# Kernel tuning notes

Measured on AMD Instinct MI355X. Metric: run time of the kernel, lower is better.

## Reference

```python
import jax, jax.numpy as jnp
import numpy as np

T, N, E = 4, 40000, 640000
D_IN, D_HID, D_OUT, NCLASS = 256, 256, 256, 2
NEG = 0.2  # leaky_relu negative slope (both GATv2 internal and outer activations)


def segment_softmax(logits, seg, n):
    m = jax.ops.segment_max(logits, seg, num_segments=n)
    ex = jnp.exp(logits - m[seg])
    s = jax.ops.segment_sum(ex, seg, num_segments=n)
    return ex / s[seg]


def gatv2(x, src, dst, Wl, Wr, bl, br, att, bias, n):
    # PyG GATv2Conv, heads=1, concat: lin_l on source, lin_r on target,
    # e = att . leaky_relu(xl_j + xr_i), softmax over incoming edges of i,
    # out_i = sum_j alpha_ij * xl_j + bias. Self-loops already appended.
    xl = x @ Wl + bl                                   # [n, C]
    xr = x @ Wr + br                                   # [n, C]
    e = jax.nn.leaky_relu(xl[src] + xr[dst], NEG)      # [E', C]
    alpha = segment_softmax(e @ att, dst, n)           # [E']
    out = jax.ops.segment_sum(alpha[:, None] * xl[src], dst, num_segments=n)
    return out + bias


def setup_inputs() -> dict:
    key = jax.random.key(0)
    ks = jax.random.split(key, 18)
    w = lambda k, shape, fan: (jax.random.normal(k, shape, dtype=jnp.float32) / np.sqrt(fan)).astype(jnp.float32)
    return {
        "fts": jax.random.normal(ks[0], (T, N, D_IN), dtype=jnp.float32),
        "graph": jax.random.randint(ks[1], (T, 2, E), 0, N, dtype=jnp.int32),
        "Wl0": w(ks[2], (D_IN, D_HID), D_IN),
        "Wr0": w(ks[3], (D_IN, D_HID), D_IN),
        "bl0": jnp.zeros((D_HID,), jnp.float32),
        "br0": jnp.zeros((D_HID,), jnp.float32),
        "att0": w(ks[4], (D_HID,), D_HID),
        "b0": jnp.zeros((D_HID,), jnp.float32),
        "Wl1": w(ks[5], (D_HID, D_OUT), D_HID),
        "Wr1": w(ks[6], (D_HID, D_OUT), D_HID),
        "bl1": jnp.zeros((D_OUT,), jnp.float32),
        "br1": jnp.zeros((D_OUT,), jnp.float32),
        "att1": w(ks[7], (D_OUT,), D_OUT),
        "b1": jnp.zeros((D_OUT,), jnp.float32),
        "W_lin": w(ks[8], (D_OUT, NCLASS), D_OUT),
        "b_lin": jnp.zeros((NCLASS,), jnp.float32),
        "time_steps": T,
    }


def reference(fts, graph, Wl0, Wr0, bl0, br0, att0, b0,
              Wl1, Wr1, bl1, br1, att1, b1, W_lin, b_lin, time_steps):
    n = fts.shape[1]
    loops = jnp.arange(n, dtype=graph.dtype)
    # PyG add_self_loops=True: append (i, i) edges per graph used.
    src0 = jnp.concatenate([graph[0, 0], loops])
    dst0 = jnp.concatenate([graph[0, 1], loops])
    # BUG-faithful: only timestep 0 survives (y = y[0]) but the last layer
    # uses G from the LAST timestep; timesteps 1..T-1 are dead compute.
    srcL = jnp.concatenate([graph[time_steps - 1, 0], loops])
    dstL = jnp.concatenate([graph[time_steps - 1, 1], loops])
    y = jax.nn.leaky_relu(gatv2(fts[0], src0, dst0, Wl0, Wr0, bl0, br0, att0, b0, n), NEG)
    y = jax.nn.leaky_relu(gatv2(y, srcL, dstL, Wl1, Wr1, bl1, br1, att1, b1, n), NEG)
    # dropout is identity in eval mode
    y = y @ W_lin + b_lin
    return jax.nn.log_softmax(y, axis=1)  # [N, nclass]
```

## Files before the change

kernel.cpp:

```cpp
#include <hip/hip_runtime.h>
#include <hip/hip_bf16.h>
#include <math.h>

#define NEG 0.2f
#define NB_MAX 256
#define CAP 5120

typedef float f32x4 __attribute__((ext_vector_type(4)));
typedef _Float16 f16;
typedef _Float16 f16x2 __attribute__((ext_vector_type(2)));
typedef _Float16 f16x8 __attribute__((ext_vector_type(8)));

#if defined(__has_builtin)
#if __has_builtin(__builtin_amdgcn_fdot2)
#define HAVE_FDOT2 1
#endif
#endif

typedef __attribute__((address_space(3))) void as3_void;
typedef __attribute__((address_space(1))) const void as1_void;

__device__ __forceinline__ void gl_lds16(const void* g, void* l) {
    __builtin_amdgcn_global_load_lds((as1_void*)g, (as3_void*)l, 16, 0, 0);
}

__global__ __launch_bounds__(256) void convert_w2(const float* __restrict__ Wl0,
                                                  const float* __restrict__ Wr0,
                                                  const float* __restrict__ Wl1,
                                                  const float* __restrict__ Wr1,
                                                  _Float16* __restrict__ Wt,
                                                  int* __restrict__ bkt_next, int nb2) {
    int l = blockIdx.y;
    int idx = blockIdx.x * blockDim.x + threadIdx.x;
    int n = idx >> 8, k = idx & 255;
    const float* Wl = l ? Wl1 : Wl0;
    const float* Wr = l ? Wr1 : Wr0;
    float v = (n < 256) ? Wl[k * 256 + n] : Wr[k * 256 + (n - 256)];
    Wt[(size_t)l * 512 * 256 + idx] = (_Float16)v;
    if (blockIdx.x == 0 && l == 0)
        for (int i = threadIdx.x; i < nb2; i += 256) bkt_next[i] = 0;
}

__device__ __forceinline__ void stage16(const _Float16* __restrict__ src,
                                        int row_base, int row_max, int k0,
                                        char* lds, int tid) {
#pragma unroll
    for (int q = 0; q < 2; ++q) {
        int off = q * 4096 + tid * 16;
        int row = off >> 6;
        int slot = (off >> 4) & 3;
        int se = slot ^ (row & 3);
        int grow = row_base + row;
        if (grow > row_max) grow = row_max;
        gl_lds16(src + (size_t)grow * 256 + k0 + se * 8,
                 lds + q * 4096 + (tid >> 6) * 1024);
    }
}

__device__ __forceinline__ void stage16_f32(const float* __restrict__ X,
                                            int row_base, int row_max, int k0,
                                            char* lds, int tid) {
#pragma unroll
    for (int u = 0; u < 4; ++u) {
        int unit = u * 256 + tid;
        int r = unit >> 3, hu = unit & 7;
        int slot = hu >> 1, sub = (hu & 1) * 8;
        int se = slot ^ (r & 3);
        int grow = row_base + r;
        if (grow > row_max) grow = row_max;
        float4 v = *(const float4*)(X + (size_t)grow * 256 + k0 + se * 8 + (hu & 1) * 4);
        f16x2 p0 = {(f16)v.x, (f16)v.y};
        f16x2 p1 = {(f16)v.z, (f16)v.w};
        uint2 w;
        w.x = __builtin_bit_cast(unsigned, p0);
        w.y = __builtin_bit_cast(unsigned, p1);
        *(uint2*)(lds + r * 64 + slot * 16 + sub) = w;
    }
}

template <int SRC>
__device__ __forceinline__ void gemm_body(char* smem, int b,
                                          const float* __restrict__ Xf,
                                          const _Float16* __restrict__ X16,
                                          const _Float16* __restrict__ Wt,
                                          const float* __restrict__ bl,
                                          const float* __restrict__ br,
                                          _Float16* __restrict__ Af,
                                          _Float16* __restrict__ Bf, int M) {
    int Mb = (M + 127) >> 7;
    int cx = b & 7, rr = b >> 3;
    int m_blk = (rr >> 2) * 8 + cx;
    int n_blk = rr & 3;
    if (m_blk >= Mb) return;
    int tid = threadIdx.x;
    int wave = tid >> 6, lane = tid & 63;
    int m0 = m_blk * 128;
    int wr = wave >> 1, wc = wave & 1;
    int r15 = lane & 15, c = lane >> 4;

    f32x4 acc[4][4];
#pragma unroll
    for (int mf = 0; mf < 4; ++mf)
#pragma unroll
        for (int nf = 0; nf < 4; ++nf) acc[mf][nf] = (f32x4){0.f, 0.f, 0.f, 0.f};

    auto stageX = [&](int k0, char* dst) {
        if constexpr (SRC == 0) stage16_f32(Xf, m0, M - 1, k0, dst, tid);
        else                    stage16(X16, m0, M - 1, k0, dst, tid);
    };

    stageX(0, smem);
    stage16(Wt, n_blk * 128, 511, 0, smem + 8192, tid);
    __syncthreads();

    for (int t = 0; t < 8; ++t) {
        int buf = t & 1;
        if (t < 7) {
            char* nb2 = smem + (buf ^ 1) * 16384;
            stageX((t + 1) * 32, nb2);
            stage16(Wt, n_blk * 128, 511, (t + 1) * 32, nb2 + 8192, tid);
        }
        const char* At = smem + buf * 16384;
        const char* Bt = At + 8192;
        f16x8 af[4], bf[4];
#pragma unroll
        for (int f = 0; f < 4; ++f) {
            int ar = wr * 64 + f * 16 + r15;
            af[f] = *(const f16x8*)(At + ar * 64 + ((c ^ (ar & 3)) << 4));
            int br_ = wc * 64 + f * 16 + r15;
            bf[f] = *(const f16x8*)(Bt + br_ * 64 + ((c ^ (br_ & 3)) << 4));
        }
#pragma unroll
        for (int mf = 0; mf < 4; ++mf)
#pragma unroll
            for (int nf = 0; nf < 4; ++nf)
                acc[mf][nf] = __builtin_amdgcn_mfma_f32_16x16x32_f16(af[mf], bf[nf], acc[mf][nf], 0, 0, 0);
        __syncthreads();
    }

    int q4 = (lane >> 4) * 4;
#pragma unroll
    for (int nf = 0; nf < 4; ++nf) {
        int n_abs = n_blk * 128 + wc * 64 + nf * 16 + r15;
        bool left = n_abs < 256;
        float bb = left ? bl[n_abs] : br[n_abs - 256];
        int col = n_abs & 255;
#pragma unroll
        for (int mf = 0; mf < 4; ++mf) {
            int rowb = m0 + wr * 64 + mf * 16 + q4;
#pragma unroll
            for (int j = 0; j < 4; ++j) {
                int row = rowb + j;
                if (row < M) {
                    float v = acc[mf][nf][j] + bb;
                    if (left) Af[(size_t)row * 256 + col] = (_Float16)v;
                    else      Bf[(size_t)row * 256 + col] = (_Float16)v;
                }
            }
        }
    }
}

__global__ __launch_bounds__(256) void binA(const int* __restrict__ src0,
                                            const int* __restrict__ dst0,
                                            const int* __restrict__ src1,
                                            const int* __restrict__ dst1,
                                            int Ereal, int EP, int nb,
                                            int* __restrict__ bkt_next,
                                            unsigned* __restrict__ bucketBuf) {
    __shared__ int hist[NB_MAX], base[NB_MAX], ofs[NB_MAX];
    int l = blockIdx.y;
    for (int i = threadIdx.x; i < nb; i += 256) hist[i] = 0;
    __syncthreads();
    const int* src = l ? src1 : src0;
    const int* dst = l ? dst1 : dst0;
    int c0 = blockIdx.x * 4096;
    int dcache[16];
#pragma unroll
    for (int k = 0; k < 16; ++k) {
        int i = c0 + k * 256 + threadIdx.x;
        int d = -1;
        if (i < EP) d = (i < Ereal) ? dst[i] : (i - Ereal);
        dcache[k] = d;
        if (d >= 0) atomicAdd(&hist[d >> 8], 1);
    }
    __syncthreads();
    for (int i = threadIdx.x; i < nb; i += 256) {
        base[i] = hist[i] ? atomicAdd(&bkt_next[l * nb + i], hist[i]) : 0;
        ofs[i] = 0;
    }
    __syncthreads();
#pragma unroll
    for (int k = 0; k < 16; ++k) {
        int i = c0 + k * 256 + threadIdx.x;
        int d = dcache[k];
        if (d >= 0) {
            int s = (i < Ereal) ? src[i] : (i - Ereal);
            int bk = d >> 8;
            int pos = base[bk] + atomicAdd(&ofs[bk], 1);
            bucketBuf[(size_t)(l * nb + bk) * CAP + pos] = (unsigned)s | ((unsigned)(d & 255) << 16);
        }
    }
}

__global__ __launch_bounds__(256) void binB_gemm0(const unsigned* __restrict__ bucketBuf,
                                                  const int* __restrict__ bkt_cnt,
                                                  int nb, int N,
                                                  int* __restrict__ beg,
                                                  int* __restrict__ end_,
                                                  unsigned short* __restrict__ csr16,
                                                  const float* __restrict__ Xf,
                                                  const _Float16* __restrict__ Wt,
                                                  const float* __restrict__ bl,
                                                  const float* __restrict__ br,
                                                  _Float16* __restrict__ Af,
                                                  _Float16* __restrict__ Bf, int M) {
    __shared__ char smem[32768];
    int blk = blockIdx.x;
    if (blk < 2 * nb) {
        int* hist = (int*)smem;
        int* sh   = (int*)(smem + 1024);
        int* nxt  = (int*)(smem + 2048);
        int l = blk / nb, b = blk % nb, t = threadIdx.x;
        int cnt = bkt_cnt[l * nb + b];
        const unsigned* buf = bucketBuf + (size_t)(l * nb + b) * CAP;
        unsigned short* csrL = csr16 + (size_t)l * nb * CAP;
        hist[t] = 0;
        __syncthreads();
        for (int i = t; i < cnt; i += 256)
            atomicAdd(&hist[buf[i] >> 16], 1);
        __syncthreads();
        int h = hist[t];
        sh[t] = h;
        __syncthreads();
        for (int o = 1; o < 256; o <<= 1) {
            int x = (t >= o) ? sh[t - o] : 0;
            __syncthreads();
            sh[t] += x;
            __syncthreads();
        }
        int excl = sh[t] - h;
        nxt[t] = excl;
        int d = b * 256 + t;
        if (d < N) {
            beg[(size_t)l * N + d] = b * CAP + excl;
            end_[(size_t)l * N + d] = b * CAP + excl + h;
        }
        __syncthreads();
        for (int i = t; i < cnt; i += 256) {
            unsigned v = buf[i];
            int pos = b * CAP + atomicAdd(&nxt[v >> 16], 1);
            csrL[pos] = (unsigned short)(v & 0xFFFFu);
        }
        return;
    }
    gemm_body<0>(smem, blk - 2 * nb, Xf, nullptr, Wt, bl, br, Af, Bf, M);
}

__global__ __launch_bounds__(256) void mfma_gemm1(const _Float16* __restrict__ X16,
                                                  const _Float16* __restrict__ Wt,
                                                  const float* __restrict__ bl,
                                                  const float* __restrict__ br,
                                                  _Float16* __restrict__ Af,
                                                  _Float16* __restrict__ Bf, int M) {
    __shared__ char smem[32768];
    gemm_body<1>(smem, blockIdx.x, nullptr, X16, Wt, bl, br, Af, Bf, M);
}

template <int MODE>
__global__ __launch_bounds__(256) void gat_node(const _Float16* __restrict__ xl,
                                                const _Float16* __restrict__ xr,
                                                const int* __restrict__ beg_,
                                                const int* __restrict__ end_,
                                                const unsigned short* __restrict__ csr,
                                                const float* __restrict__ att,
                                                const float* __restrict__ bias,
                                                _Float16* __restrict__ y16,
                                                const float* __restrict__ Wlin,
                                                const float* __restrict__ blin,
                                                float* __restrict__ out, int n) {
    int wid = (int)((blockIdx.x * (size_t)blockDim.x + threadIdx.x) >> 6);
    int lane = threadIdx.x & 63;
    if (wid >= n) return;
    int g = lane >> 5, li = lane & 31;
    int beg = beg_[wid], end = end_[wid];

    f16x8 xr8 = ((const f16x8*)(xr + (size_t)wid * 256))[li];
    float4 t0 = ((const float4*)att)[li * 2];
    float4 t1 = ((const float4*)att)[li * 2 + 1];
    f16x2 t01 = {(f16)t0.x, (f16)t0.y}, t23 = {(f16)t0.z, (f16)t0.w};
    f16x2 t45 = {(f16)t1.x, (f16)t1.y}, t67 = {(f16)t1.z, (f16)t1.w};
    const f16 ng = (f16)NEG;
    const f16x8 n8 = {ng, ng, ng, ng, ng, ng, ng, ng};

    float m = -INFINITY, ssum = 0.f;
    float acc[8] = {0.f, 0.f, 0.f, 0.f, 0.f, 0.f, 0.f, 0.f};

    auto step = [&](f16x8 a, bool valid) {
        f16x8 v = a + xr8;
        f16x8 lk = __builtin_elementwise_max(v, v * n8);
#ifdef HAVE_FDOT2
        f16x2 q;
        q[0] = lk[0]; q[1] = lk[1];
        float dot = __builtin_amdgcn_fdot2(q, t01, 0.f, false);
        q[0] = lk[2]; q[1] = lk[3];
        dot = __builtin_amdgcn_fdot2(q, t23, dot, false);
        q[0] = lk[4]; q[1] = lk[5];
        dot = __builtin_amdgcn_fdot2(q, t45, dot, false);
        q[0] = lk[6]; q[1] = lk[7];
        dot = __builtin_amdgcn_fdot2(q, t67, dot, false);
#else
        float dot = (float)lk[0] * (float)t01[0] + (float)lk[1] * (float)t01[1] +
                    (float)lk[2] * (float)t23[0] + (float)lk[3] * (float)t23[1] +
                    (float)lk[4] * (float)t45[0] + (float)lk[5] * (float)t45[1] +
                    (float)lk[6] * (float)t67[0] + (float)lk[7] * (float)t67[1];
#endif
#pragma unroll
        for (int off = 16; off > 0; off >>= 1) dot += __shfl_xor(dot, off);
        if (valid) {
            if (dot > m + 8.f) {
                float sc = __expf(m - dot);
                ssum = ssum * sc + 1.f;
#pragma unroll
                for (int i = 0; i < 8; ++i) acc[i] = acc[i] * sc + (float)a[i];
                m = dot;
            } else {
                float p = __expf(dot - m);
                ssum += p;
#pragma unroll
                for (int i = 0; i < 8; ++i) acc[i] += p * (float)a[i];
            }
        }
    };

    int j = beg;
    for (; j + 16 <= end; j += 16) {
        f16x8 a[8];
#pragma unroll
        for (int u = 0; u < 8; ++u) {
            int s = csr[j + 2 * u + g];
            a[u] = ((const f16x8*)(xl + (size_t)s * 256))[li];
        }
#pragma unroll
        for (int u = 0; u < 8; ++u) step(a[u], true);
    }
    if (j + 8 <= end) {
        f16x8 a[4];
#pragma unroll
        for (int u = 0; u < 4; ++u) {
            int s = csr[j + 2 * u + g];
            a[u] = ((const f16x8*)(xl + (size_t)s * 256))[li];
        }
#pragma unroll
        for (int u = 0; u < 4; ++u) step(a[u], true);
        j += 8;
    }
    for (; j < end; j += 2) {
        int e = j + g;
        int s = csr[e < end ? e : end - 1];
        f16x8 a = ((const f16x8*)(xl + (size_t)s * 256))[li];
        step(a, e < end);
    }

    float m_o = __shfl_xor(m, 32);
    float s_o = __shfl_xor(ssum, 32);
    float ms = fmaxf(m, m_o);
    float wa = __expf(m - ms), wb = __expf(m_o - ms);
    float inv = 1.f / (ssum * wa + s_o * wb);
    float4 bb0 = ((const float4*)bias)[li * 2];
    float4 bb1 = ((const float4*)bias)[li * 2 + 1];
    float bbv[8] = {bb0.x, bb0.y, bb0.z, bb0.w, bb1.x, bb1.y, bb1.z, bb1.w};
    float o8[8];
#pragma unroll
    for (int i = 0; i < 8; ++i) {
        float ao = __shfl_xor(acc[i], 32);
        float o = (acc[i] * wa + ao * wb) * inv + bbv[i];
        o8[i] = o > 0.f ? o : NEG * o;
    }

    if (MODE == 0) {
        if (g == 0) {
            f16x8 w;
#pragma unroll
            for (int i = 0; i < 8; ++i) w[i] = (f16)o8[i];
            ((f16x8*)(y16 + (size_t)wid * 256))[li] = w;
        }
    } else {
        float z0 = 0.f, z1 = 0.f;
#pragma unroll
        for (int p = 0; p < 4; ++p) {
            float4 q = ((const float4*)Wlin)[li * 4 + p];
            z0 += o8[2 * p] * q.x + o8[2 * p + 1] * q.z;
            z1 += o8[2 * p] * q.y + o8[2 * p + 1] * q.w;
        }
#pragma unroll
        for (int off = 16; off > 0; off >>= 1) {
            z0 += __shfl_xor(z0, off);
            z1 += __shfl_xor(z1, off);
        }
        if (lane == 0) {
            z0 += blin[0];
            z1 += blin[1];
            float mx = fmaxf(z0, z1);
            float lse = mx + logf(expf(z0 - mx) + expf(z1 - mx));
            out[(size_t)wid * 2 + 0] = z0 - lse;
            out[(size_t)wid * 2 + 1] = z1 - lse;
        }
    }
}

extern "C" void kernel_launch(void* const* d_in, const int* in_sizes, int n_in,
                              void* d_out, int out_size, void* d_ws, size_t ws_size,
                              hipStream_t stream) {
    const float* fts   = (const float*)d_in[0];
    const int*   graph = (const int*)d_in[1];
    const float* Wl0 = (const float*)d_in[2];
    const float* Wr0 = (const float*)d_in[3];
    const float* bl0 = (const float*)d_in[4];
    const float* br0 = (const float*)d_in[5];
    const float* att0 = (const float*)d_in[6];
    const float* b0  = (const float*)d_in[7];
    const float* Wl1 = (const float*)d_in[8];
    const float* Wr1 = (const float*)d_in[9];
    const float* bl1 = (const float*)d_in[10];
    const float* br1 = (const float*)d_in[11];
    const float* att1 = (const float*)d_in[12];
    const float* b1  = (const float*)d_in[13];
    const float* Wlin = (const float*)d_in[14];
    const float* blin = (const float*)d_in[15];

    int N = out_size / 2;
    long T = in_sizes[0] / ((long)N * 256);
    long E = in_sizes[1] / (2 * T);
    int EP = (int)E + N;
    int nb = (N + 255) / 256;

    char* ws = (char*)d_ws;
    size_t off = 0;
    auto alloc = [&](size_t bytes) -> void* {
        void* p = ws + off;
        off += (bytes + 255) & ~(size_t)255;
        return p;
    };
    _Float16* Af  = (_Float16*)alloc((size_t)N * 256 * 2);
    _Float16* Bf  = (_Float16*)alloc((size_t)N * 256 * 2);
    _Float16* Y16 = (_Float16*)alloc((size_t)N * 256 * 2);
    _Float16* Wt  = (_Float16*)alloc((size_t)2 * 512 * 256 * 2);
    int* beg      = (int*)alloc((size_t)2 * N * 4);
    int* end_     = (int*)alloc((size_t)2 * N * 4);
    unsigned short* csr16 = (unsigned short*)alloc((size_t)2 * nb * CAP * 2);
    unsigned* bucketBuf = (unsigned*)alloc((size_t)2 * nb * CAP * 4);
    int* bkt_next = (int*)alloc((size_t)2 * nb * 4);
    (void)ws_size; (void)n_in;

    int Mb = (N + 127) / 128;
    int gemm_blocks = ((Mb + 7) / 8) * 8 * 4;
    dim3 chunk_grid((EP + 4095) / 4096, 2);
    int node_blocks = (N + 3) / 4;

    const int* src0 = graph;
    const int* dst0 = graph + E;
    const int* srcL = graph + (T - 1) * 2 * E;
    const int* dstL = graph + (T - 1) * 2 * E + E;

    convert_w2<<<dim3(512, 2), 256, 0, stream>>>(Wl0, Wr0, Wl1, Wr1, Wt, bkt_next, 2 * nb);
    binA<<<chunk_grid, 256, 0, stream>>>(src0, dst0, srcL, dstL, (int)E, EP, nb,
                                         bkt_next, bucketBuf);
    binB_gemm0<<<2 * nb + gemm_blocks, 256, 0, stream>>>(bucketBuf, bkt_next, nb, N,
                                                         beg, end_, csr16,
                                                         fts, Wt, bl0, br0, Af, Bf, N);
    gat_node<0><<<node_blocks, 256, 0, stream>>>(Af, Bf, beg, end_, csr16, att0, b0,
                                                 Y16, nullptr, nullptr, nullptr, N);
    mfma_gemm1<<<gemm_blocks, 256, 0, stream>>>(Y16, Wt + (size_t)512 * 256,
                                                bl1, br1, Af, Bf, N);
    gat_node<1><<<node_blocks, 256, 0, stream>>>(Af, Bf, beg + N, end_ + N,
                                                 csr16 + (size_t)nb * CAP, att1, b1,
                                                 nullptr, Wlin, blin, (float*)d_out, N);
}
```

Baseline: 232.6 us.

## Split layer-0 aggregation and overlap its tail with layer-1 GEMM

Layer-0 node aggregation is split into two launches. The second launch co-schedules the remaining nodes with layer-1 GEMM tiles over rows already finished, and a separate launch handles the leftover GEMM tiles. Layer-1 outputs go to new buffers so the GEMM no longer overwrites xl/xr while aggregation still reads them. The weight conversion is merged into the binning kernel and the counter zeroing moves to a memset. Non-temporal loads and stores are also used for xr and y16. This adds launches and workspace, and the co-scheduled kernel mixes block types with different resource needs.

```diff
diff --git a/kernel.cpp b/kernel.cpp
--- a/kernel.cpp
+++ b/kernel.cpp
@@ -10,6 +10,7 @@
 typedef _Float16 f16;
 typedef _Float16 f16x2 __attribute__((ext_vector_type(2)));
 typedef _Float16 f16x8 __attribute__((ext_vector_type(8)));
+typedef unsigned u32x4 __attribute__((ext_vector_type(4)));
 
 #if defined(__has_builtin)
 #if __has_builtin(__builtin_amdgcn_fdot2)
@@ -24,21 +25,12 @@
     __builtin_amdgcn_global_load_lds((as1_void*)g, (as3_void*)l, 16, 0, 0);
 }
 
-__global__ __launch_bounds__(256) void convert_w2(const float* __restrict__ Wl0,
-                                                  const float* __restrict__ Wr0,
-                                                  const float* __restrict__ Wl1,
-                                                  const float* __restrict__ Wr1,
-                                                  _Float16* __restrict__ Wt,
-                                                  int* __restrict__ bkt_next, int nb2) {
-    int l = blockIdx.y;
-    int idx = blockIdx.x * blockDim.x + threadIdx.x;
-    int n = idx >> 8, k = idx & 255;
-    const float* Wl = l ? Wl1 : Wl0;
-    const float* Wr = l ? Wr1 : Wr0;
-    float v = (n < 256) ? Wl[k * 256 + n] : Wr[k * 256 + (n - 256)];
-    Wt[(size_t)l * 512 * 256 + idx] = (_Float16)v;
-    if (blockIdx.x == 0 && l == 0)
-        for (int i = threadIdx.x; i < nb2; i += 256) bkt_next[i] = 0;
+__device__ __forceinline__ f16x8 nt_load8(const _Float16* p) {
+    u32x4 v = __builtin_nontemporal_load((const u32x4*)p);
+    return __builtin_bit_cast(f16x8, v);
+}
+__device__ __forceinline__ void nt_store8(_Float16* p, f16x8 w) {
+    __builtin_nontemporal_store(__builtin_bit_cast(u32x4, w), (u32x4*)p);
 }
 
 __device__ __forceinline__ void stage16(const _Float16* __restrict__ src,
@@ -79,7 +71,7 @@
 }
 
 template <int SRC>
-__device__ __forceinline__ void gemm_body(char* smem, int b,
+__device__ __forceinline__ void gemm_body(char* smem, int b, int m_base, int m_tiles,
                                           const float* __restrict__ Xf,
                                           const _Float16* __restrict__ X16,
                                           const _Float16* __restrict__ Wt,
@@ -87,14 +79,13 @@
                                           const float* __restrict__ br,
                                           _Float16* __restrict__ Af,
                                           _Float16* __restrict__ Bf, int M) {
-    int Mb = (M + 127) >> 7;
     int cx = b & 7, rr = b >> 3;
-    int m_blk = (rr >> 2) * 8 + cx;
+    int ml = (rr >> 2) * 8 + cx;
     int n_blk = rr & 3;
-    if (m_blk >= Mb) return;
+    if (ml >= m_tiles) return;
     int tid = threadIdx.x;
     int wave = tid >> 6, lane = tid & 63;
-    int m0 = m_blk * 128;
+    int m0 = (m_base + ml) * 128;
     int wr = wave >> 1, wc = wave & 1;
     int r15 = lane & 15, c = lane >> 4;
 
@@ -161,20 +152,177 @@
     }
 }
 
-__global__ __launch_bounds__(256) void binA(const int* __restrict__ src0,
-                                            const int* __restrict__ dst0,
-                                            const int* __restrict__ src1,
-                                            const int* __restrict__ dst1,
-                                            int Ereal, int EP, int nb,
-                                            int* __restrict__ bkt_next,
-                                            unsigned* __restrict__ bucketBuf) {
+template <int MODE>
+__device__ __forceinline__ void gat_body(int wid, int lane,
+                                         const _Float16* __restrict__ xl,
+                                         const _Float16* __restrict__ xr,
+                                         const int* __restrict__ beg_,
+                                         const int* __restrict__ end_,
+                                         const unsigned short* __restrict__ csr,
+                                         const float* __restrict__ att,
+                                         const float* __restrict__ bias,
+                                         _Float16* __restrict__ y16,
+                                         const float* __restrict__ Wlin,
+                                         const float* __restrict__ blin,
+                                         float* __restrict__ out) {
+    int g = lane >> 5, li = lane & 31;
+    int beg = beg_[wid], end = end_[wid];
+
+    f16x8 xr8 = nt_load8(xr + (size_t)wid * 256 + li * 8);
+    float4 t0 = ((const float4*)att)[li * 2];
+    float4 t1 = ((const float4*)att)[li * 2 + 1];
+    f16x2 t01 = {(f16)t0.x, (f16)t0.y}, t23 = {(f16)t0.z, (f16)t0.w};
+    f16x2 t45 = {(f16)t1.x, (f16)t1.y}, t67 = {(f16)t1.z, (f16)t1.w};
+    const f16 ng = (f16)NEG;
+    const f16x8 n8 = {ng, ng, ng, ng, ng, ng, ng, ng};
+
+    float m = -INFINITY, ssum = 0.f;
+    float acc[8] = {0.f, 0.f, 0.f, 0.f, 0.f, 0.f, 0.f, 0.f};
+
+    auto step = [&](f16x8 a, bool valid) {
+        f16x8 v = a + xr8;
+        f16x8 lk = __builtin_elementwise_max(v, v * n8);
+#ifdef HAVE_FDOT2
+        f16x2 q;
+        q[0] = lk[0]; q[1] = lk[1];
+        float dot = __builtin_amdgcn_fdot2(q, t01, 0.f, false);
+        q[0] = lk[2]; q[1] = lk[3];
+        dot = __builtin_amdgcn_fdot2(q, t23, dot, false);
+        q[0] = lk[4]; q[1] = lk[5];
+        dot = __builtin_amdgcn_fdot2(q, t45, dot, false);
+        q[0] = lk[6]; q[1] = lk[7];
+        dot = __builtin_amdgcn_fdot2(q, t67, dot, false);
+#else
+        float dot = (float)lk[0] * (float)t01[0] + (float)lk[1] * (float)t01[1] +
+                    (float)lk[2] * (float)t23[0] + (float)lk[3] * (float)t23[1] +
+                    (float)lk[4] * (float)t45[0] + (float)lk[5] * (float)t45[1] +
+                    (float)lk[6] * (float)t67[0] + (float)lk[7] * (float)t67[1];
+#endif
+#pragma unroll
+        for (int off = 16; off > 0; off >>= 1) dot += __shfl_xor(dot, off);
+        if (valid) {
+            if (dot > m + 8.f) {
+                float sc = __expf(m - dot);
+                ssum = ssum * sc + 1.f;
+#pragma unroll
+                for (int i = 0; i < 8; ++i) acc[i] = acc[i] * sc + (float)a[i];
+                m = dot;
+            } else {
+                float p = __expf(dot - m);
+                ssum += p;
+#pragma unroll
+                for (int i = 0; i < 8; ++i) acc[i] += p * (float)a[i];
+            }
+        }
+    };
+
+    int j = beg;
+    for (; j + 16 <= end; j += 16) {
+        f16x8 a[8];
+#pragma unroll
+        for (int u = 0; u < 8; ++u) {
+            int s = csr[j + 2 * u + g];
+            a[u] = ((const f16x8*)(xl + (size_t)s * 256))[li];
+        }
+#pragma unroll
+        for (int u = 0; u < 8; ++u) step(a[u], true);
+    }
+    if (j + 8 <= end) {
+        f16x8 a[4];
+#pragma unroll
+        for (int u = 0; u < 4; ++u) {
+            int s = csr[j + 2 * u + g];
+            a[u] = ((const f16x8*)(xl + (size_t)s * 256))[li];
+        }
+#pragma unroll
+        for (int u = 0; u < 4; ++u) step(a[u], true);
+        j += 8;
+    }
+    for (; j < end; j += 2) {
+        int e = j + g;
+        int s = csr[e < end ? e : end - 1];
+        f16x8 a = ((const f16x8*)(xl + (size_t)s * 256))[li];
+        step(a, e < end);
+    }
+
+    float m_o = __shfl_xor(m, 32);
+    float s_o = __shfl_xor(ssum, 32);
+    float ms = fmaxf(m, m_o);
+    float wa = __expf(m - ms), wb = __expf(m_o - ms);
+    float inv = 1.f / (ssum * wa + s_o * wb);
+    float4 bb0 = ((const float4*)bias)[li * 2];
+    float4 bb1 = ((const float4*)bias)[li * 2 + 1];
+    float bbv[8] = {bb0.x, bb0.y, bb0.z, bb0.w, bb1.x, bb1.y, bb1.z, bb1.w};
+    float o8[8];
+#pragma unroll
+    for (int i = 0; i < 8; ++i) {
+        float ao = __shfl_xor(acc[i], 32);
+        float o = (acc[i] * wa + ao * wb) * inv + bbv[i];
+        o8[i] = o > 0.f ? o : NEG * o;
+    }
+
+    if (MODE == 0) {
+        if (g == 0) {
+            f16x8 w;
+#pragma unroll
+            for (int i = 0; i < 8; ++i) w[i] = (f16)o8[i];
+            nt_store8(y16 + (size_t)wid * 256 + li * 8, w);
+        }
+    } else {
+        float z0 = 0.f, z1 = 0.f;
+#pragma unroll
+        for (int p = 0; p < 4; ++p) {
+            float4 q = ((const float4*)Wlin)[li * 4 + p];
+            z0 += o8[2 * p] * q.x + o8[2 * p + 1] * q.z;
+            z1 += o8[2 * p] * q.y + o8[2 * p + 1] * q.w;
+        }
+#pragma unroll
+        for (int off = 16; off > 0; off >>= 1) {
+            z0 += __shfl_xor(z0, off);
+            z1 += __shfl_xor(z1, off);
+        }
+        if (lane == 0) {
+            z0 += blin[0];
+            z1 += blin[1];
+            float mx = fmaxf(z0, z1);
+            float lse = mx + logf(expf(z0 - mx) + expf(z1 - mx));
+            out[(size_t)wid * 2 + 0] = z0 - lse;
+            out[(size_t)wid * 2 + 1] = z1 - lse;
+        }
+    }
+}
+
+__global__ __launch_bounds__(256) void conv_binA(const int* __restrict__ src0,
+                                                 const int* __restrict__ dst0,
+                                                 const int* __restrict__ src1,
+                                                 const int* __restrict__ dst1,
+                                                 int Ereal, int EP, int nb, int binAx,
+                                                 int* __restrict__ bkt_next,
+                                                 unsigned* __restrict__ bucketBuf,
+                                                 const float* __restrict__ Wl0,
+                                                 const float* __restrict__ Wr0,
+                                                 const float* __restrict__ Wl1,
+                                                 const float* __restrict__ Wr1,
+                                                 _Float16* __restrict__ Wt) {
+    int blk = blockIdx.x;
+    if (blk >= 2 * binAx) {
+        int cb = blk - 2 * binAx;
+        int l = cb >> 9;
+        int idx = (cb & 511) * 256 + threadIdx.x;
+        int n = idx >> 8, k = idx & 255;
+        const float* Wl = l ? Wl1 : Wl0;
+        const float* Wr = l ? Wr1 : Wr0;
+        float v = (n < 256) ? Wl[k * 256 + n] : Wr[k * 256 + (n - 256)];
+        Wt[(size_t)l * 512 * 256 + idx] = (_Float16)v;
+        return;
+    }
     __shared__ int hist[NB_MAX], base[NB_MAX], ofs[NB_MAX];
-    int l = blockIdx.y;
+    int l = blk / binAx;
+    int c0 = (blk % binAx) * 4096;
     for (int i = threadIdx.x; i < nb; i += 256) hist[i] = 0;
     __syncthreads();
     const int* src = l ? src1 : src0;
     const int* dst = l ? dst1 : dst0;
-    int c0 = blockIdx.x * 4096;
     int dcache[16];
 #pragma unroll
     for (int k = 0; k < 16; ++k) {
@@ -214,7 +362,8 @@
                                                   const float* __restrict__ bl,
                                                   const float* __restrict__ br,
                                                   _Float16* __restrict__ Af,
-                                                  _Float16* __restrict__ Bf, int M) {
+                                                  _Float16* __restrict__ Bf,
+                                                  int M, int m_tiles) {
     __shared__ char smem[32768];
     int blk = blockIdx.x;
     if (blk < 2 * nb) {
@@ -254,159 +403,75 @@
         }
         return;
     }
-    gemm_body<0>(smem, blk - 2 * nb, Xf, nullptr, Wt, bl, br, Af, Bf, M);
-}
-
-__global__ __launch_bounds__(256) void mfma_gemm1(const _Float16* __restrict__ X16,
-                                                  const _Float16* __restrict__ Wt,
-                                                  const float* __restrict__ bl,
-                                                  const float* __restrict__ br,
-                                                  _Float16* __restrict__ Af,
-                                                  _Float16* __restrict__ Bf, int M) {
+    gemm_body<0>(smem, blk - 2 * nb, 0, m_tiles, Xf, nullptr, Wt, bl, br, Af, Bf, M);
+}
+
+__global__ __launch_bounds__(256) void gat0_A(const _Float16* __restrict__ xl,
+                                              const _Float16* __restrict__ xr,
+                                              const int* __restrict__ beg_,
+                                              const int* __restrict__ end_,
+                                              const unsigned short* __restrict__ csr,
+                                              const float* __restrict__ att,
+                                              const float* __restrict__ bias,
+                                              _Float16* __restrict__ y16, int H) {
+    int wid = (int)((blockIdx.x * (size_t)blockDim.x + threadIdx.x) >> 6);
+    if (wid >= H) return;
+    gat_body<0>(wid, threadIdx.x & 63, xl, xr, beg_, end_, csr, att, bias,
+                y16, nullptr, nullptr, nullptr);
+}
+
+__global__ __launch_bounds__(256) void gat0B_gemm1A(const _Float16* __restrict__ xl,
+                                                    const _Float16* __restrict__ xr,
+                                                    const int* __restrict__ beg_,
+                                                    const int* __restrict__ end_,
+                                                    const unsigned short* __restrict__ csr,
+                                                    const float* __restrict__ att,
+                                                    const float* __restrict__ bias,
+                                                    _Float16* __restrict__ y16,
+                                                    int H, int n, int nbB,
+                                                    const _Float16* __restrict__ Wt1,
+                                                    const float* __restrict__ bl1,
+                                                    const float* __restrict__ br1,
+                                                    _Float16* __restrict__ Af2,
+                                                    _Float16* __restrict__ Bf2,
+                                                    int m_tilesA) {
     __shared__ char smem[32768];
-    gemm_body<1>(smem, blockIdx.x, nullptr, X16, Wt, bl, br, Af, Bf, M);
-}
-
-template <int MODE>
-__global__ __launch_bounds__(256) void gat_node(const _Float16* __restrict__ xl,
-                                                const _Float16* __restrict__ xr,
-                                                const int* __restrict__ beg_,
-                                                const int* __restrict__ end_,
-                                                const unsigned short* __restrict__ csr,
-                                                const float* __restrict__ att,
-                                                const float* __restrict__ bias,
-                                                _Float16* __restrict__ y16,
-                                                const float* __restrict__ Wlin,
-                                                const float* __restrict__ blin,
-                                                float* __restrict__ out, int n) {
+    int blk = blockIdx.x;
+    if (blk < nbB) {
+        int wid = H + (int)(((size_t)blk * blockDim.x + threadIdx.x) >> 6);
+        if (wid >= n) return;
+        gat_body<0>(wid, threadIdx.x & 63, xl, xr, beg_, end_, csr, att, bias,
+                    y16, nullptr, nullptr, nullptr);
+        return;
+    }
+    gemm_body<1>(smem, blk - nbB, 0, m_tilesA, nullptr, y16, Wt1, bl1, br1, Af2, Bf2, n);
+}
+
+__global__ __launch_bounds__(256) void gemm1_B(const _Float16* __restrict__ X16,
+                                               const _Float16* __restrict__ Wt,
+                                               const float* __restrict__ bl,
+                                               const float* __restrict__ br,
+                                               _Float16* __restrict__ Af,
+                                               _Float16* __restrict__ Bf,
+                                               int M, int m_base, int m_tiles) {
+    __shared__ char smem[32768];
+    gemm_body<1>(smem, blockIdx.x, m_base, m_tiles, nullptr, X16, Wt, bl, br, Af, Bf, M);
+}
+
+__global__ __launch_bounds__(256) void gat1(const _Float16* __restrict__ xl,
+                                            const _Float16* __restrict__ xr,
+                                            const int* __restrict__ beg_,
+                                            const int* __restrict__ end_,
+                                            const unsigned short* __restrict__ csr,
+                                            const float* __restrict__ att,
+                                            const float* __restrict__ bias,
+                                            const float* __restrict__ Wlin,
+                                            const float* __restrict__ blin,
+                                            float* __restrict__ out, int n) {
     int wid = (int)((blockIdx.x * (size_t)blockDim.x + threadIdx.x) >> 6);
-    int lane = threadIdx.x & 63;
     if (wid >= n) return;
-    int g = lane >> 5, li = lane & 31;
-    int beg = beg_[wid], end = end_[wid];
-
-    f16x8 xr8 = ((const f16x8*)(xr + (size_t)wid * 256))[li];
-    float4 t0 = ((const float4*)att)[li * 2];
-    float4 t1 = ((const float4*)att)[li * 2 + 1];
-    f16x2 t01 = {(f16)t0.x, (f16)t0.y}, t23 = {(f16)t0.z, (f16)t0.w};
-    f16x2 t45 = {(f16)t1.x, (f16)t1.y}, t67 = {(f16)t1.z, (f16)t1.w};
-    const f16 ng = (f16)NEG;
-    const f16x8 n8 = {ng, ng, ng, ng, ng, ng, ng, ng};
-
-    float m = -INFINITY, ssum = 0.f;
-    float acc[8] = {0.f, 0.f, 0.f, 0.f, 0.f, 0.f, 0.f, 0.f};
-
-    auto step = [&](f16x8 a, bool valid) {
-        f16x8 v = a + xr8;
-        f16x8 lk = __builtin_elementwise_max(v, v * n8);
-#ifdef HAVE_FDOT2
-        f16x2 q;
-        q[0] = lk[0]; q[1] = lk[1];
-        float dot = __builtin_amdgcn_fdot2(q, t01, 0.f, false);
-        q[0] = lk[2]; q[1] = lk[3];
-        dot = __builtin_amdgcn_fdot2(q, t23, dot, false);
-        q[0] = lk[4]; q[1] = lk[5];
-        dot = __builtin_amdgcn_fdot2(q, t45, dot, false);
-        q[0] = lk[6]; q[1] = lk[7];
-        dot = __builtin_amdgcn_fdot2(q, t67, dot, false);
-#else
-        float dot = (float)lk[0] * (float)t01[0] + (float)lk[1] * (float)t01[1] +
-                    (float)lk[2] * (float)t23[0] + (float)lk[3] * (float)t23[1] +
-                    (float)lk[4] * (float)t45[0] + (float)lk[5] * (float)t45[1] +
-                    (float)lk[6] * (float)t67[0] + (float)lk[7] * (float)t67[1];
-#endif
-#pragma unroll
-        for (int off = 16; off > 0; off >>= 1) dot += __shfl_xor(dot, off);
-        if (valid) {
-            if (dot > m + 8.f) {
-                float sc = __expf(m - dot);
-                ssum = ssum * sc + 1.f;
-#pragma unroll
-                for (int i = 0; i < 8; ++i) acc[i] = acc[i] * sc + (float)a[i];
-                m = dot;
-            } else {
-                float p = __expf(dot - m);
-                ssum += p;
-#pragma unroll
-                for (int i = 0; i < 8; ++i) acc[i] += p * (float)a[i];
-            }
-        }
-    };
-
-    int j = beg;
-    for (; j + 16 <= end; j += 16) {
-        f16x8 a[8];
-#pragma unroll
-        for (int u = 0; u < 8; ++u) {
-            int s = csr[j + 2 * u + g];
-            a[u] = ((const f16x8*)(xl + (size_t)s * 256))[li];
-        }
-#pragma unroll
-        for (int u = 0; u < 8; ++u) step(a[u], true);
-    }
-    if (j + 8 <= end) {
-        f16x8 a[4];
-#pragma unroll
-        for (int u = 0; u < 4; ++u) {
-            int s = csr[j + 2 * u + g];
-            a[u] = ((const f16x8*)(xl + (size_t)s * 256))[li];
-        }
-#pragma unroll
-        for (int u = 0; u < 4; ++u) step(a[u], true);
-        j += 8;
-    }
-    for (; j < end; j += 2) {
-        int e = j + g;
-        int s = csr[e < end ? e : end - 1];
-        f16x8 a = ((const f16x8*)(xl + (size_t)s * 256))[li];
-        step(a, e < end);
-    }
-
-    float m_o = __shfl_xor(m, 32);
-    float s_o = __shfl_xor(ssum, 32);
-    float ms = fmaxf(m, m_o);
-    float wa = __expf(m - ms), wb = __expf(m_o - ms);
-    float inv = 1.f / (ssum * wa + s_o * wb);
-    float4 bb0 = ((const float4*)bias)[li * 2];
-    float4 bb1 = ((const float4*)bias)[li * 2 + 1];
-    float bbv[8] = {bb0.x, bb0.y, bb0.z, bb0.w, bb1.x, bb1.y, bb1.z, bb1.w};
-    float o8[8];
-#pragma unroll
-    for (int i = 0; i < 8; ++i) {
-        float ao = __shfl_xor(acc[i], 32);
-        float o = (acc[i] * wa + ao * wb) * inv + bbv[i];
-        o8[i] = o > 0.f ? o : NEG * o;
-    }
-
-    if (MODE == 0) {
-        if (g == 0) {
-            f16x8 w;
-#pragma unroll
-            for (int i = 0; i < 8; ++i) w[i] = (f16)o8[i];
-            ((f16x8*)(y16 + (size_t)wid * 256))[li] = w;
-        }
-    } else {
-        float z0 = 0.f, z1 = 0.f;
-#pragma unroll
-        for (int p = 0; p < 4; ++p) {
-            float4 q = ((const float4*)Wlin)[li * 4 + p];
-            z0 += o8[2 * p] * q.x + o8[2 * p + 1] * q.z;
-            z1 += o8[2 * p] * q.y + o8[2 * p + 1] * q.w;
-        }
-#pragma unroll
-        for (int off = 16; off > 0; off >>= 1) {
-            z0 += __shfl_xor(z0, off);
-            z1 += __shfl_xor(z1, off);
-        }
-        if (lane == 0) {
-            z0 += blin[0];
-            z1 += blin[1];
-            float mx = fmaxf(z0, z1);
-            float lse = mx + logf(expf(z0 - mx) + expf(z1 - mx));
-            out[(size_t)wid * 2 + 0] = z0 - lse;
-            out[(size_t)wid * 2 + 1] = z1 - lse;
-        }
-    }
+    gat_body<1>(wid, threadIdx.x & 63, xl, xr, beg_, end_, csr, att, bias,
+                nullptr, Wlin, blin, out);
 }
 
 extern "C" void kernel_launch(void* const* d_in, const int* in_sizes, int n_in,
@@ -444,6 +509,8 @@
     };
     _Float16* Af  = (_Float16*)alloc((size_t)N * 256 * 2);
     _Float16* Bf  = (_Float16*)alloc((size_t)N * 256 * 2);
+    _Float16* Af2 = (_Float16*)alloc((size_t)N * 256 * 2);
+    _Float16* Bf2 = (_Float16*)alloc((size_t)N * 256 * 2);
     _Float16* Y16 = (_Float16*)alloc((size_t)N * 256 * 2);
     _Float16* Wt  = (_Float16*)alloc((size_t)2 * 512 * 256 * 2);
     int* beg      = (int*)alloc((size_t)2 * N * 4);
@@ -454,8 +521,15 @@
     (void)ws_size; (void)n_in;
 
     int Mb = (N + 127) / 128;
-    int gemm_blocks = ((Mb + 7) / 8) * 8 * 4;
-    dim3 chunk_grid((EP + 4095) / 4096, 2);
+    int MbA = (Mb * 3 / 4) & ~7;
+    int H = MbA * 128;
+    int gemm_blocks  = ((Mb + 7) / 8) * 8 * 4;
+    int gemmA_blocks = MbA * 4;
+    int MbBcnt = Mb - MbA;
+    int gemmB_blocks = ((MbBcnt + 7) / 8) * 8 * 4;
+    int binAx = (EP + 4095) / 4096;
+    int gat0A_blocks = (H + 3) / 4;
+    int gat0B_blocks = (N - H + 3) / 4;
     int node_blocks = (N + 3) / 4;
 
     const int* src0 = graph;
@@ -463,17 +537,21 @@
     const int* srcL = graph + (T - 1) * 2 * E;
     const int* dstL = graph + (T - 1) * 2 * E + E;
 
-    convert_w2<<<dim3(512, 2), 256, 0, stream>>>(Wl0, Wr0, Wl1, Wr1, Wt, bkt_next, 2 * nb);
-    binA<<<chunk_grid, 256, 0, stream>>>(src0, dst0, srcL, dstL, (int)E, EP, nb,
-                                         bkt_next, bucketBuf);
+    hipMemsetAsync(bkt_next, 0, (size_t)2 * nb * 4, stream);
+    conv_binA<<<2 * binAx + 1024, 256, 0, stream>>>(src0, dst0, srcL, dstL,
+                                                    (int)E, EP, nb, binAx,
+                                                    bkt_next, bucketBuf,
+                                                    Wl0, Wr0, Wl1, Wr1, Wt);
     binB_gemm0<<<2 * nb + gemm_blocks, 256, 0, stream>>>(bucketBuf, bkt_next, nb, N,
                                                          beg, end_, csr16,
-                                                         fts, Wt, bl0, br0, Af, Bf, N);
-    gat_node<0><<<node_blocks, 256, 0, stream>>>(Af, Bf, beg, end_, csr16, att0, b0,
-                                                 Y16, nullptr, nullptr, nullptr, N);
-    mfma_gemm1<<<gemm_blocks, 256, 0, stream>>>(Y16, Wt + (size_t)512 * 256,
-                                                bl1, br1, Af, Bf, N);
-    gat_node<1><<<node_blocks, 256, 0, stream>>>(Af, Bf, beg + N, end_ + N,
-                                                 csr16 + (size_t)nb * CAP, att1, b1,
-                                                 nullptr, Wlin, blin, (float*)d_out, N);
-}
+                                                         fts, Wt, bl0, br0, Af, Bf, N, Mb);
+    gat0_A<<<gat0A_blocks, 256, 0, stream>>>(Af, Bf, beg, end_, csr16, att0, b0, Y16, H);
+    gat0B_gemm1A<<<gat0B_blocks + gemmA_blocks, 256, 0, stream>>>(
+        Af, Bf, beg, end_, csr16, att0, b0, Y16, H, N, gat0B_blocks,
+        Wt + (size_t)512 * 256, bl1, br1, Af2, Bf2, MbA);
+    gemm1_B<<<gemmB_blocks, 256, 0, stream>>>(Y16, Wt + (size_t)512 * 256,
+                                              bl1, br1, Af2, Bf2, N, MbA, MbBcnt);
+    gat1<<<node_blocks, 256, 0, stream>>>(Af2, Bf2, beg + N, end_ + N,
+                                          csr16 + (size_t)nb * CAP, att1, b1,
+                                          Wlin, blin, (float*)d_out, N);
+}
```

Measured after the change: 271.6 us. 1.17x slower.
